# Kernel tuning notes

Hardware: AMD Instinct MI355X
Metric: run time of the kernel (lower is better)

## Reference

```python
import jax, jax.numpy as jnp
import numpy as np

BATCH, SEQ, FEAT, LAYERS = 32, 512, 1024, 2


def setup_inputs() -> dict:
    key = jax.random.key(0)
    ks = jax.random.split(key, 1 + 3 * LAYERS)
    inp = {"x": jax.random.normal(ks[0], (BATCH, SEQ, FEAT), dtype=jnp.float32)}
    scale_i = 1.0 / np.sqrt(FEAT)
    for l in range(LAYERS):
        # flax OptimizedLSTMCell: input dense (no bias) + hidden dense (with bias),
        # both producing 4*features (gates i, f, g, o concatenated).
        inp[f"Wi{l}"] = jax.random.normal(ks[1 + 3 * l], (FEAT, 4 * FEAT), dtype=jnp.float32) * scale_i
        inp[f"Wh{l}"] = jax.random.normal(ks[2 + 3 * l], (FEAT, 4 * FEAT), dtype=jnp.float32) * scale_i
        inp[f"b{l}"] = jnp.zeros((4 * FEAT,), dtype=jnp.float32)
    return inp


def _lstm_layer(x, Wi, Wh, b):
    # x: [B, T, F_in]; returns [B, T, F]
    B = x.shape[0]
    F = Wh.shape[0]
    # Precompute input projections for all steps (one big GEMM): [B, T, 4F]
    xz = jnp.einsum("btf,fg->btg", x, Wi) + b

    def step(carry, xz_t):
        c, h = carry
        z = xz_t + h @ Wh  # [B, 4F]
        i, f, g, o = jnp.split(z, 4, axis=-1)
        c_new = jax.nn.sigmoid(f) * c + jax.nn.sigmoid(i) * jnp.tanh(g)
        h_new = jax.nn.sigmoid(o) * jnp.tanh(c_new)
        return (c_new, h_new), h_new

    init = (jnp.zeros((B, F), x.dtype), jnp.zeros((B, F), x.dtype))
    _, ys = jax.lax.scan(step, init, jnp.swapaxes(xz, 0, 1))  # scan over time
    return jnp.swapaxes(ys, 0, 1)


def reference(x, Wi0, Wh0, b0, Wi1, Wh1, b1):
    y = _lstm_layer(x, Wi0, Wh0, b0)
    y = _lstm_layer(y, Wi1, Wh1, b1)
    return y
```

## Files before the change

kernel.cpp:

```cpp
#include <hip/hip_runtime.h>
#include <hip/hip_bf16.h>
#include <hip/hip_fp16.h>


typedef _Float16 f16x8 __attribute__((ext_vector_type(8)));
typedef __fp16 fp16x2 __attribute__((ext_vector_type(2)));
typedef float f32x4 __attribute__((ext_vector_type(4)));

#define NB 32
#define NTT 512
#define NF 1024
#define NG 4096
#define TFE (NTT * NF)
#define NWG 256
#define NTHR 512

#define W_F16X8 8192
#define W_BYTES (W_F16X8 * 16)
#define ZQSEG 33
#define Z_FLOATS (8 * 16 * ZQSEG)
#define LDS_BYTES (W_BYTES + Z_FLOATS * 4)
#define RINGB 65536
#define DEPTH 8
#define MBOX 4096

#define LOG2E 1.44269504f

__device__ __forceinline__ float sigm(float v) {
  return __builtin_amdgcn_rcpf(1.0f + __builtin_amdgcn_exp2f(-LOG2E * v));
}
__device__ __forceinline__ float tanh_s(float v) {
  return 2.0f * __builtin_amdgcn_rcpf(1.0f + __builtin_amdgcn_exp2f(-2.0f * LOG2E * v)) - 1.0f;
}

__device__ __forceinline__ unsigned pk(float a, float b) {
  union { fp16x2 h2; unsigned u; } c;
  c.h2 = __builtin_amdgcn_cvt_pkrtz(a, b);
  return c.u;
}

__device__ __forceinline__ f16x8 cvt8(f32x4 lo, f32x4 hi) {
  union { unsigned u[4]; f16x8 h8; } u;
  u.u[0] = pk(lo[0], lo[1]);
  u.u[1] = pk(lo[2], lo[3]);
  u.u[2] = pk(hi[0], hi[1]);
  u.u[3] = pk(hi[2], hi[3]);
  return u.h8;
}

__device__ __forceinline__ void ld4(f16x8 o[4], const char* p) {
  asm volatile("global_load_dwordx4 %0, %4, off sc0 sc1\n\t"
               "global_load_dwordx4 %1, %4, off offset:64 sc0 sc1\n\t"
               "global_load_dwordx4 %2, %4, off offset:128 sc0 sc1\n\t"
               "global_load_dwordx4 %3, %4, off offset:192 sc0 sc1"
               : "=&v"(o[0]), "=&v"(o[1]), "=&v"(o[2]), "=&v"(o[3])
               : "v"(p) : "memory");
}

__global__ __launch_bounds__(NTHR, 1) void lstm_persist(
    const float* __restrict__ x,
    const float* __restrict__ Wi0, const float* __restrict__ Wh0, const float* __restrict__ bv0,
    const float* __restrict__ Wi1, const float* __restrict__ Wh1, const float* __restrict__ bv1,
    float* __restrict__ out, unsigned short* __restrict__ hring_u16,
    unsigned* __restrict__ bar) {
  extern __shared__ char lds[];
  f16x8* Wl = (f16x8*)lds;
  float* Zr = (float*)(lds + W_BYTES);

  const int wg = blockIdx.x;
  const int tid = threadIdx.x;
  const int role = wg >> 7;
  const int fg = wg & 127;
  const int fbase = fg * 8;
  const int w = tid >> 6;
  const int Kq = w >> 1;
  const int mt = w & 1;
  const int lane = tid & 63;
  const int lr = lane & 15;
  const int g = lane >> 4;
  const bool master = (fg == 0);
  unsigned gen = 0;

  auto arrive = [&]() {
    asm volatile("s_waitcnt vmcnt(0) lgkmcnt(0)" ::: "memory");
    __syncthreads();
    ++gen;
    if (tid == 0)
      asm volatile("global_store_dword %0, %1, off sc0 sc1"
                   :: "v"(&bar[wg * 16]), "v"(gen) : "memory");
    if (master) {
      if (tid < 64) {
        const unsigned* fa = &bar[(role * 128 + 2 * tid) * 16];
        const unsigned* fb = &bar[(role * 128 + 2 * tid + 1) * 16];
        asm volatile("L%=:\n\t"
                     "global_load_dword v20, %0, off sc0 sc1\n\t"
                     "global_load_dword v21, %1, off sc0 sc1\n\t"
                     "s_waitcnt vmcnt(0)\n\t"
                     "v_cmp_lt_u32 vcc, v20, %2\n\t"
                     "s_mov_b64 s[14:15], vcc\n\t"
                     "v_cmp_lt_u32 vcc, v21, %2\n\t"
                     "s_or_b64 vcc, vcc, s[14:15]\n\t"
                     "s_cbranch_vccnz L%="
                     :: "v"(fa), "v"(fb), "v"(gen)
                     : "memory", "v20", "v21", "vcc", "s14", "s15");
      }
      __syncthreads();
      if (tid < 256)
        asm volatile("global_store_dword %0, %1, off sc0 sc1"
                     :: "v"(&bar[MBOX + tid * 16 + role]), "v"(gen) : "memory");
    }
  };

  auto waitAB = [&](unsigned minA, unsigned minB) {
    const unsigned* mb = &bar[MBOX + wg * 16];
    asm volatile("L%=:\n\t"
                 "global_load_dwordx2 v[20:21], %0, off sc0 sc1\n\t"
                 "s_waitcnt vmcnt(0)\n\t"
                 "v_cmp_lt_u32 vcc, v20, %1\n\t"
                 "s_mov_b64 s[14:15], vcc\n\t"
                 "v_cmp_lt_u32 vcc, v21, %2\n\t"
                 "s_or_b64 vcc, vcc, s[14:15]\n\t"
                 "s_cbranch_vccnz L%="
                 :: "v"(mb), "v"(minA), "v"(minB)
                 : "memory", "v20", "v21", "vcc", "s14", "s15");
  };

  const float* Wi = role ? Wi1 : Wi0;
  const float* Wh = role ? Wh1 : Wh0;
  const float* bv = role ? bv1 : bv0;
  char* h0b = (char*)hring_u16;
  char* h1b = (char*)hring_u16 + DEPTH * RINGB;
  unsigned* hmine = (unsigned*)(role ? h1b : h0b);

  for (int idx = tid; idx < 16384; idx += NTHR) {
    const int k = idx >> 3, chunk = idx & 7;
    const int q = chunk >> 1, half = chunk & 1;
    const float* src = (k < NF) ? (Wi + (size_t)k * NG) : (Wh + (size_t)(k - NF) * NG);
    const f32x4 v = *(const f32x4*)(src + q * NF + fbase + half * 4);
    const int s = k >> 5, kg = (k >> 3) & 3, jj = k & 7;
#pragma unroll
    for (int j = 0; j < 4; ++j) {
      const int c = q * 8 + half * 4 + j;
      _Float16* dst = (_Float16*)&Wl[((s * 2 + (c >> 4)) * 64) + kg * 16 + (c & 15)];
      dst[jj] = (_Float16)v[j];
    }
  }
  if (tid < 128) {
    const int b = tid >> 2, fp = tid & 3;
    __hip_atomic_store(&hmine[b * 512 + (fbase >> 1) + fp], 0u,
                       __ATOMIC_RELAXED, __HIP_MEMORY_SCOPE_AGENT);
  }
  float bias[4][2];
  if (tid < 128) {
    const int fp = tid & 3;
#pragma unroll
    for (int q = 0; q < 4; ++q) {
      bias[q][0] = bv[q * NF + fbase + 2 * fp];
      bias[q][1] = bv[q * NF + fbase + 2 * fp + 1];
    }
  }
  float cst[2] = {0.f, 0.f};
  __syncthreads();
  arrive();
  waitAB(1, 1);

  const int nrounds = role ? (NTT + 3) : NTT;
  for (int rd = 0; rd < nrounds; ++rd) {
    const bool doit = role == 0 ? true : (rd >= 3);
    const int t = role == 0 ? rd : rd - 3;

    if (doit) {
      f32x4 acc0 = {0.f, 0.f, 0.f, 0.f}, acc1 = {0.f, 0.f, 0.f, 0.f};
      const int brow = mt * 16 + lr;

      if (role == 0 && w < 4) {
        const float* xp = x + (size_t)brow * TFE + (size_t)t * NF + Kq * 512 + g * 8;
#pragma unroll
        for (int ks = 0; ks < 16; ++ks) {
          const int s = Kq * 16 + ks;
          const f32x4 al = *(const f32x4*)(xp + ks * 32);
          const f32x4 ah = *(const f32x4*)(xp + ks * 32 + 4);
          const f16x8 A = cvt8(al, ah);
          acc0 = __builtin_amdgcn_mfma_f32_16x16x32_f16(A, Wl[(s * 2 + 0) * 64 + lane], acc0, 0, 0, 0);
          acc1 = __builtin_amdgcn_mfma_f32_16x16x32_f16(A, Wl[(s * 2 + 1) * 64 + lane], acc1, 0, 0, 0);
        }
      } else {
        unsigned minA = 0, minB = 0;
        const char* hp;
        if (role == 0) {
          minA = rd + 1;
          minB = (rd >= 4) ? (unsigned)(rd - 3) : 0u;
          hp = h0b + (size_t)(rd & 7) * RINGB + brow * 2048
               + ((Kq - 2) * 512 + g * 8) * 2;
        } else if (Kq < 2) {
          minA = rd - 1;
          hp = h0b + (size_t)((rd - 2) & 7) * RINGB + brow * 2048
               + (Kq * 512 + g * 8) * 2;
        } else {
          minB = (rd == 3) ? 1u : (unsigned)(rd + 1);
          hp = h1b + (size_t)((rd - 3) & 7) * RINGB + brow * 2048
               + ((Kq - 2) * 512 + g * 8) * 2;
        }
        waitAB(minA, minB);

        f16x8 T[16];
        ld4(T + 0, hp);       ld4(T + 4, hp + 256);
        ld4(T + 8, hp + 512); ld4(T + 12, hp + 768);
        asm volatile("s_waitcnt vmcnt(12)" ::: "memory");
        __builtin_amdgcn_sched_barrier(0);
#pragma unroll
        for (int kk = 0; kk < 4; ++kk) {
          const int s = Kq * 16 + kk;
          acc0 = __builtin_amdgcn_mfma_f32_16x16x32_f16(T[kk], Wl[(s * 2 + 0) * 64 + lane], acc0, 0, 0, 0);
          acc1 = __builtin_amdgcn_mfma_f32_16x16x32_f16(T[kk], Wl[(s * 2 + 1) * 64 + lane], acc1, 0, 0, 0);
        }
        asm volatile("s_waitcnt vmcnt(8)" ::: "memory");
        __builtin_amdgcn_sched_barrier(0);
#pragma unroll
        for (int kk = 0; kk < 4; ++kk) {
          const int s = Kq * 16 + 4 + kk;
          acc0 = __builtin_amdgcn_mfma_f32_16x16x32_f16(T[4 + kk], Wl[(s * 2 + 0) * 64 + lane], acc0, 0, 0, 0);
          acc1 = __builtin_amdgcn_mfma_f32_16x16x32_f16(T[4 + kk], Wl[(s * 2 + 1) * 64 + lane], acc1, 0, 0, 0);
        }
        asm volatile("s_waitcnt vmcnt(4)" ::: "memory");
        __builtin_amdgcn_sched_barrier(0);
#pragma unroll
        for (int kk = 0; kk < 4; ++kk) {
          const int s = Kq * 16 + 8 + kk;
          acc0 = __builtin_amdgcn_mfma_f32_16x16x32_f16(T[8 + kk], Wl[(s * 2 + 0) * 64 + lane], acc0, 0, 0, 0);
          acc1 = __builtin_amdgcn_mfma_f32_16x16x32_f16(T[8 + kk], Wl[(s * 2 + 1) * 64 + lane], acc1, 0, 0, 0);
        }
        asm volatile("s_waitcnt vmcnt(0)" ::: "memory");
        __builtin_amdgcn_sched_barrier(0);
#pragma unroll
        for (int kk = 0; kk < 4; ++kk) {
          const int s = Kq * 16 + 12 + kk;
          acc0 = __builtin_amdgcn_mfma_f32_16x16x32_f16(T[12 + kk], Wl[(s * 2 + 0) * 64 + lane], acc0, 0, 0, 0);
          acc1 = __builtin_amdgcn_mfma_f32_16x16x32_f16(T[12 + kk], Wl[(s * 2 + 1) * 64 + lane], acc1, 0, 0, 0);
        }
      }

      {
        float* zb = Zr + (size_t)w * 16 * ZQSEG;
#pragma unroll
        for (int reg = 0; reg < 4; ++reg) {
          zb[(g * 4 + reg) * ZQSEG + lr] = acc0[reg];
          zb[(g * 4 + reg) * ZQSEG + 16 + lr] = acc1[reg];
        }
      }
    }
    __syncthreads();

    if (doit && tid < 128) {
      const int b = tid >> 2, fp = tid & 3;
      const int bmt = b >> 4, row = b & 15;
      float hv[2];
#pragma unroll
      for (int e = 0; e < 2; ++e) {
        const int f = 2 * fp + e;
        float zq[4];
#pragma unroll
        for (int q = 0; q < 4; ++q) {
          const int c = q * 8 + f;
          float sum = bias[q][e];
#pragma unroll
          for (int kq = 0; kq < 4; ++kq)
            sum += Zr[((kq * 2 + bmt) * 16 + row) * ZQSEG + c];
          zq[q] = sum;
        }
        const float cn = sigm(zq[1]) * cst[e] + sigm(zq[0]) * tanh_s(zq[2]);
        hv[e] = sigm(zq[3]) * tanh_s(cn);
        cst[e] = cn;
      }
      const int wslot = (t + 1) & 7;
      __hip_atomic_store(&hmine[(size_t)wslot * (RINGB / 4) + b * 512 + (fbase >> 1) + fp],
                         pk(hv[0], hv[1]), __ATOMIC_RELAXED, __HIP_MEMORY_SCOPE_AGENT);
      if (role == 1)
        *(float2*)(out + (size_t)b * TFE + (size_t)t * NF + fbase + 2 * fp) =
            make_float2(hv[0], hv[1]);
    }
    arrive();
  }
}

extern "C" void kernel_launch(void* const* d_in, const int* in_sizes, int n_in,
                              void* d_out, int out_size, void* d_ws, size_t ws_size,
                              hipStream_t stream) {
  (void)in_sizes; (void)n_in; (void)out_size; (void)ws_size;
  const float* x   = (const float*)d_in[0];
  const float* Wi0 = (const float*)d_in[1];
  const float* Wh0 = (const float*)d_in[2];
  const float* b0  = (const float*)d_in[3];
  const float* Wi1 = (const float*)d_in[4];
  const float* Wh1 = (const float*)d_in[5];
  const float* b1  = (const float*)d_in[6];
  float* out = (float*)d_out;

  unsigned short* hring = (unsigned short*)d_ws;
  unsigned* bar = (unsigned*)((char*)d_ws + 2 * DEPTH * RINGB);

  (void)hipMemsetAsync(bar, 0, 32768, stream);

  (void)hipFuncSetAttribute((const void*)lstm_persist,
                            hipFuncAttributeMaxDynamicSharedMemorySize, LDS_BYTES);

  lstm_persist<<<dim3(NWG), dim3(NTHR), LDS_BYTES, stream>>>(
      x, Wi0, Wh0, b0, Wi1, Wh1, b1, out, hring, bar);
}
```

Before: 3.782 ms.

## Shrink workgroups to two waves, drop LDS reduction and per-wave barriers

Workgroups drop from 512 to 128 threads. Each wave now covers the full K range for its 16 batch rows instead of splitting K across four waves, which removes the LDS partial-sum reduction and the __syncthreads inside each step. The gate nonlinearity runs directly on MFMA accumulators, using a lane shuffle to pair the gate columns, and h is written back as fp16 shorts. Barrier arrival becomes per wave, so the master polls 256 flags per role. Each wave now does four times the serial MFMA chain and loads per step, which lengthens per-step latency on the critical recurrent path.

```diff
diff --git a/kernel.cpp b/kernel.cpp
--- a/kernel.cpp
+++ b/kernel.cpp
@@ -13,17 +13,13 @@
 #define NG 4096
 #define TFE (NTT * NF)
 #define NWG 256
-#define NTHR 512
-
-#define W_F16X8 8192
-#define W_BYTES (W_F16X8 * 16)
-#define ZQSEG 33
-#define Z_FLOATS (8 * 16 * ZQSEG)
-#define LDS_BYTES (W_BYTES + Z_FLOATS * 4)
+#define NTHR 128
+
+#define W_BYTES 131072
+#define LDS_BYTES W_BYTES
 #define RINGB 65536
 #define DEPTH 8
-#define MBOX 4096
-
+#define MBOX 8192
 #define LOG2E 1.44269504f
 
 __device__ __forceinline__ float sigm(float v) {
@@ -65,49 +61,50 @@
     unsigned* __restrict__ bar) {
   extern __shared__ char lds[];
   f16x8* Wl = (f16x8*)lds;
-  float* Zr = (float*)(lds + W_BYTES);
 
   const int wg = blockIdx.x;
   const int tid = threadIdx.x;
   const int role = wg >> 7;
   const int fg = wg & 127;
   const int fbase = fg * 8;
-  const int w = tid >> 6;
-  const int Kq = w >> 1;
-  const int mt = w & 1;
+  const int mt = tid >> 6;
   const int lane = tid & 63;
-  const int lr = lane & 15;
+  const int n = lane & 15;
   const int g = lane >> 4;
-  const bool master = (fg == 0);
   unsigned gen = 0;
 
   auto arrive = [&]() {
     asm volatile("s_waitcnt vmcnt(0) lgkmcnt(0)" ::: "memory");
-    __syncthreads();
     ++gen;
-    if (tid == 0)
+    if (lane == 0)
       asm volatile("global_store_dword %0, %1, off sc0 sc1"
-                   :: "v"(&bar[wg * 16]), "v"(gen) : "memory");
-    if (master) {
-      if (tid < 64) {
-        const unsigned* fa = &bar[(role * 128 + 2 * tid) * 16];
-        const unsigned* fb = &bar[(role * 128 + 2 * tid + 1) * 16];
-        asm volatile("L%=:\n\t"
-                     "global_load_dword v20, %0, off sc0 sc1\n\t"
-                     "global_load_dword v21, %1, off sc0 sc1\n\t"
-                     "s_waitcnt vmcnt(0)\n\t"
-                     "v_cmp_lt_u32 vcc, v20, %2\n\t"
-                     "s_mov_b64 s[14:15], vcc\n\t"
-                     "v_cmp_lt_u32 vcc, v21, %2\n\t"
-                     "s_or_b64 vcc, vcc, s[14:15]\n\t"
-                     "s_cbranch_vccnz L%="
-                     :: "v"(fa), "v"(fb), "v"(gen)
-                     : "memory", "v20", "v21", "vcc", "s14", "s15");
-      }
-      __syncthreads();
-      if (tid < 256)
+                   :: "v"(&bar[(wg * 2 + mt) * 16]), "v"(gen) : "memory");
+    if (fg == 0 && mt == 0) {
+      const unsigned* f0 = &bar[(role * 256 + lane * 4 + 0) * 16];
+      const unsigned* f1 = &bar[(role * 256 + lane * 4 + 1) * 16];
+      const unsigned* f2 = &bar[(role * 256 + lane * 4 + 2) * 16];
+      const unsigned* f3 = &bar[(role * 256 + lane * 4 + 3) * 16];
+      asm volatile("L%=:\n\t"
+                   "global_load_dword v20, %0, off sc0 sc1\n\t"
+                   "global_load_dword v21, %1, off sc0 sc1\n\t"
+                   "global_load_dword v22, %2, off sc0 sc1\n\t"
+                   "global_load_dword v23, %3, off sc0 sc1\n\t"
+                   "s_waitcnt vmcnt(0)\n\t"
+                   "v_cmp_lt_u32 vcc, v20, %4\n\t"
+                   "s_mov_b64 s[14:15], vcc\n\t"
+                   "v_cmp_lt_u32 vcc, v21, %4\n\t"
+                   "s_or_b64 s[14:15], vcc, s[14:15]\n\t"
+                   "v_cmp_lt_u32 vcc, v22, %4\n\t"
+                   "s_or_b64 s[14:15], vcc, s[14:15]\n\t"
+                   "v_cmp_lt_u32 vcc, v23, %4\n\t"
+                   "s_or_b64 vcc, vcc, s[14:15]\n\t"
+                   "s_cbranch_vccnz L%="
+                   :: "v"(f0), "v"(f1), "v"(f2), "v"(f3), "v"(gen)
+                   : "memory", "v20", "v21", "v22", "v23", "vcc", "s14", "s15");
+#pragma unroll
+      for (int j = 0; j < 4; ++j)
         asm volatile("global_store_dword %0, %1, off sc0 sc1"
-                     :: "v"(&bar[MBOX + tid * 16 + role]), "v"(gen) : "memory");
+                     :: "v"(&bar[MBOX + (lane * 4 + j) * 16 + role]), "v"(gen) : "memory");
     }
   };
 
@@ -130,7 +127,7 @@
   const float* bv = role ? bv1 : bv0;
   char* h0b = (char*)hring_u16;
   char* h1b = (char*)hring_u16 + DEPTH * RINGB;
-  unsigned* hmine = (unsigned*)(role ? h1b : h0b);
+  char* hmine = role ? h1b : h0b;
 
   for (int idx = tid; idx < 16384; idx += NTHR) {
     const int k = idx >> 3, chunk = idx & 7;
@@ -145,24 +142,56 @@
       dst[jj] = (_Float16)v[j];
     }
   }
-  if (tid < 128) {
+  {
     const int b = tid >> 2, fp = tid & 3;
-    __hip_atomic_store(&hmine[b * 512 + (fbase >> 1) + fp], 0u,
+    __hip_atomic_store((unsigned*)hmine + b * 512 + (fbase >> 1) + fp, 0u,
                        __ATOMIC_RELAXED, __HIP_MEMORY_SCOPE_AGENT);
   }
-  float bias[4][2];
-  if (tid < 128) {
-    const int fp = tid & 3;
-#pragma unroll
-    for (int q = 0; q < 4; ++q) {
-      bias[q][0] = bv[q * NF + fbase + 2 * fp];
-      bias[q][1] = bv[q * NF + fbase + 2 * fp + 1];
-    }
-  }
-  float cst[2] = {0.f, 0.f};
+  float bq[4];
+#pragma unroll
+  for (int q = 0; q < 4; ++q) bq[q] = bv[q * NF + fbase + (lane & 7)];
+  float cst[4] = {0.f, 0.f, 0.f, 0.f};
   __syncthreads();
   arrive();
   waitAB(1, 1);
+
+  auto hphase = [&](const char* hp, int sbase, f32x4& a0, f32x4& a1) {
+    f16x8 T[32];
+#pragma unroll
+    for (int q = 0; q < 8; ++q) ld4(T + q * 4, hp + q * 256);
+    asm volatile("s_waitcnt vmcnt(24)" ::: "memory");
+    __builtin_amdgcn_sched_barrier(0);
+#pragma unroll
+    for (int kk = 0; kk < 8; ++kk) {
+      const int s = sbase + kk;
+      a0 = __builtin_amdgcn_mfma_f32_16x16x32_f16(T[kk], Wl[(s * 2 + 0) * 64 + lane], a0, 0, 0, 0);
+      a1 = __builtin_amdgcn_mfma_f32_16x16x32_f16(T[kk], Wl[(s * 2 + 1) * 64 + lane], a1, 0, 0, 0);
+    }
+    asm volatile("s_waitcnt vmcnt(16)" ::: "memory");
+    __builtin_amdgcn_sched_barrier(0);
+#pragma unroll
+    for (int kk = 8; kk < 16; ++kk) {
+      const int s = sbase + kk;
+      a0 = __builtin_amdgcn_mfma_f32_16x16x32_f16(T[kk], Wl[(s * 2 + 0) * 64 + lane], a0, 0, 0, 0);
+      a1 = __builtin_amdgcn_mfma_f32_16x16x32_f16(T[kk], Wl[(s * 2 + 1) * 64 + lane], a1, 0, 0, 0);
+    }
+    asm volatile("s_waitcnt vmcnt(8)" ::: "memory");
+    __builtin_amdgcn_sched_barrier(0);
+#pragma unroll
+    for (int kk = 16; kk < 24; ++kk) {
+      const int s = sbase + kk;
+      a0 = __builtin_amdgcn_mfma_f32_16x16x32_f16(T[kk], Wl[(s * 2 + 0) * 64 + lane], a0, 0, 0, 0);
+      a1 = __builtin_amdgcn_mfma_f32_16x16x32_f16(T[kk], Wl[(s * 2 + 1) * 64 + lane], a1, 0, 0, 0);
+    }
+    asm volatile("s_waitcnt vmcnt(0)" ::: "memory");
+    __builtin_amdgcn_sched_barrier(0);
+#pragma unroll
+    for (int kk = 24; kk < 32; ++kk) {
+      const int s = sbase + kk;
+      a0 = __builtin_amdgcn_mfma_f32_16x16x32_f16(T[kk], Wl[(s * 2 + 0) * 64 + lane], a0, 0, 0, 0);
+      a1 = __builtin_amdgcn_mfma_f32_16x16x32_f16(T[kk], Wl[(s * 2 + 1) * 64 + lane], a1, 0, 0, 0);
+    }
+  };
 
   const int nrounds = role ? (NTT + 3) : NTT;
   for (int rd = 0; rd < nrounds; ++rd) {
@@ -170,114 +199,55 @@
     const int t = role == 0 ? rd : rd - 3;
 
     if (doit) {
-      f32x4 acc0 = {0.f, 0.f, 0.f, 0.f}, acc1 = {0.f, 0.f, 0.f, 0.f};
-      const int brow = mt * 16 + lr;
-
-      if (role == 0 && w < 4) {
-        const float* xp = x + (size_t)brow * TFE + (size_t)t * NF + Kq * 512 + g * 8;
-#pragma unroll
-        for (int ks = 0; ks < 16; ++ks) {
-          const int s = Kq * 16 + ks;
+      f32x4 a0 = {0.f, 0.f, 0.f, 0.f}, a1 = {0.f, 0.f, 0.f, 0.f};
+      const int brow = mt * 16 + n;
+
+      if (role == 0) {
+        const float* xp = x + (size_t)brow * TFE + (size_t)t * NF + g * 8;
+#pragma unroll 8
+        for (int ks = 0; ks < 32; ++ks) {
           const f32x4 al = *(const f32x4*)(xp + ks * 32);
           const f32x4 ah = *(const f32x4*)(xp + ks * 32 + 4);
           const f16x8 A = cvt8(al, ah);
-          acc0 = __builtin_amdgcn_mfma_f32_16x16x32_f16(A, Wl[(s * 2 + 0) * 64 + lane], acc0, 0, 0, 0);
-          acc1 = __builtin_amdgcn_mfma_f32_16x16x32_f16(A, Wl[(s * 2 + 1) * 64 + lane], acc1, 0, 0, 0);
+          a0 = __builtin_amdgcn_mfma_f32_16x16x32_f16(A, Wl[(ks * 2 + 0) * 64 + lane], a0, 0, 0, 0);
+          a1 = __builtin_amdgcn_mfma_f32_16x16x32_f16(A, Wl[(ks * 2 + 1) * 64 + lane], a1, 0, 0, 0);
         }
+        const unsigned minB = (rd >= 4) ? (unsigned)(rd - 3) : 0u;
+        waitAB(rd + 1, minB);
+        hphase(h0b + (size_t)(rd & 7) * RINGB + brow * 2048 + g * 16, 32, a0, a1);
       } else {
-        unsigned minA = 0, minB = 0;
-        const char* hp;
-        if (role == 0) {
-          minA = rd + 1;
-          minB = (rd >= 4) ? (unsigned)(rd - 3) : 0u;
-          hp = h0b + (size_t)(rd & 7) * RINGB + brow * 2048
-               + ((Kq - 2) * 512 + g * 8) * 2;
-        } else if (Kq < 2) {
-          minA = rd - 1;
-          hp = h0b + (size_t)((rd - 2) & 7) * RINGB + brow * 2048
-               + (Kq * 512 + g * 8) * 2;
-        } else {
-          minB = (rd == 3) ? 1u : (unsigned)(rd + 1);
-          hp = h1b + (size_t)((rd - 3) & 7) * RINGB + brow * 2048
-               + ((Kq - 2) * 512 + g * 8) * 2;
-        }
-        waitAB(minA, minB);
-
-        f16x8 T[16];
-        ld4(T + 0, hp);       ld4(T + 4, hp + 256);
-        ld4(T + 8, hp + 512); ld4(T + 12, hp + 768);
-        asm volatile("s_waitcnt vmcnt(12)" ::: "memory");
-        __builtin_amdgcn_sched_barrier(0);
-#pragma unroll
-        for (int kk = 0; kk < 4; ++kk) {
-          const int s = Kq * 16 + kk;
-          acc0 = __builtin_amdgcn_mfma_f32_16x16x32_f16(T[kk], Wl[(s * 2 + 0) * 64 + lane], acc0, 0, 0, 0);
-          acc1 = __builtin_amdgcn_mfma_f32_16x16x32_f16(T[kk], Wl[(s * 2 + 1) * 64 + lane], acc1, 0, 0, 0);
-        }
-        asm volatile("s_waitcnt vmcnt(8)" ::: "memory");
-        __builtin_amdgcn_sched_barrier(0);
-#pragma unroll
-        for (int kk = 0; kk < 4; ++kk) {
-          const int s = Kq * 16 + 4 + kk;
-          acc0 = __builtin_amdgcn_mfma_f32_16x16x32_f16(T[4 + kk], Wl[(s * 2 + 0) * 64 + lane], acc0, 0, 0, 0);
-          acc1 = __builtin_amdgcn_mfma_f32_16x16x32_f16(T[4 + kk], Wl[(s * 2 + 1) * 64 + lane], acc1, 0, 0, 0);
-        }
-        asm volatile("s_waitcnt vmcnt(4)" ::: "memory");
-        __builtin_amdgcn_sched_barrier(0);
-#pragma unroll
-        for (int kk = 0; kk < 4; ++kk) {
-          const int s = Kq * 16 + 8 + kk;
-          acc0 = __builtin_amdgcn_mfma_f32_16x16x32_f16(T[8 + kk], Wl[(s * 2 + 0) * 64 + lane], acc0, 0, 0, 0);
-          acc1 = __builtin_amdgcn_mfma_f32_16x16x32_f16(T[8 + kk], Wl[(s * 2 + 1) * 64 + lane], acc1, 0, 0, 0);
-        }
-        asm volatile("s_waitcnt vmcnt(0)" ::: "memory");
-        __builtin_amdgcn_sched_barrier(0);
-#pragma unroll
-        for (int kk = 0; kk < 4; ++kk) {
-          const int s = Kq * 16 + 12 + kk;
-          acc0 = __builtin_amdgcn_mfma_f32_16x16x32_f16(T[12 + kk], Wl[(s * 2 + 0) * 64 + lane], acc0, 0, 0, 0);
-          acc1 = __builtin_amdgcn_mfma_f32_16x16x32_f16(T[12 + kk], Wl[(s * 2 + 1) * 64 + lane], acc1, 0, 0, 0);
+        waitAB(rd - 1, 0);
+        hphase(h0b + (size_t)((rd - 2) & 7) * RINGB + brow * 2048 + g * 16, 0, a0, a1);
+        const unsigned minB = (rd == 3) ? 1u : (unsigned)(rd + 1);
+        waitAB(0, minB);
+        hphase(h1b + (size_t)((rd - 3) & 7) * RINGB + brow * 2048 + g * 16, 32, a0, a1);
+      }
+
+      float o0[4], o1[4];
+#pragma unroll
+      for (int r = 0; r < 4; ++r) {
+        o0[r] = __shfl_xor(a0[r], 8, 64);
+        o1[r] = __shfl_xor(a1[r], 8, 64);
+      }
+      if (n < 8) {
+        char* hdst = hmine + (size_t)((t + 1) & 7) * RINGB;
+#pragma unroll
+        for (int r = 0; r < 4; ++r) {
+          const float zi = a0[r] + bq[0];
+          const float zf = o0[r] + bq[1];
+          const float zg = a1[r] + bq[2];
+          const float zo = o1[r] + bq[3];
+          const float cn = sigm(zf) * cst[r] + sigm(zi) * tanh_s(zg);
+          const float hv = sigm(zo) * tanh_s(cn);
+          cst[r] = cn;
+          const int b = mt * 16 + g * 4 + r;
+          const unsigned hu = pk(hv, hv);
+          asm volatile("global_store_short %0, %1, off sc0 sc1"
+                       :: "v"(hdst + b * 2048 + (fbase + n) * 2), "v"(hu) : "memory");
+          if (role == 1)
+            out[(size_t)b * TFE + (size_t)t * NF + fbase + n] = hv;
         }
       }
-
-      {
-        float* zb = Zr + (size_t)w * 16 * ZQSEG;
-#pragma unroll
-        for (int reg = 0; reg < 4; ++reg) {
-          zb[(g * 4 + reg) * ZQSEG + lr] = acc0[reg];
-          zb[(g * 4 + reg) * ZQSEG + 16 + lr] = acc1[reg];
-        }
-      }
-    }
-    __syncthreads();
-
-    if (doit && tid < 128) {
-      const int b = tid >> 2, fp = tid & 3;
-      const int bmt = b >> 4, row = b & 15;
-      float hv[2];
-#pragma unroll
-      for (int e = 0; e < 2; ++e) {
-        const int f = 2 * fp + e;
-        float zq[4];
-#pragma unroll
-        for (int q = 0; q < 4; ++q) {
-          const int c = q * 8 + f;
-          float sum = bias[q][e];
-#pragma unroll
-          for (int kq = 0; kq < 4; ++kq)
-            sum += Zr[((kq * 2 + bmt) * 16 + row) * ZQSEG + c];
-          zq[q] = sum;
-        }
-        const float cn = sigm(zq[1]) * cst[e] + sigm(zq[0]) * tanh_s(zq[2]);
-        hv[e] = sigm(zq[3]) * tanh_s(cn);
-        cst[e] = cn;
-      }
-      const int wslot = (t + 1) & 7;
-      __hip_atomic_store(&hmine[(size_t)wslot * (RINGB / 4) + b * 512 + (fbase >> 1) + fp],
-                         pk(hv[0], hv[1]), __ATOMIC_RELAXED, __HIP_MEMORY_SCOPE_AGENT);
-      if (role == 1)
-        *(float2*)(out + (size_t)b * TFE + (size_t)t * NF + fbase + 2 * fp) =
-            make_float2(hv[0], hv[1]);
     }
     arrive();
   }
@@ -299,7 +269,7 @@
   unsigned short* hring = (unsigned short*)d_ws;
   unsigned* bar = (unsigned*)((char*)d_ws + 2 * DEPTH * RINGB);
 
-  (void)hipMemsetAsync(bar, 0, 32768, stream);
+  (void)hipMemsetAsync(bar, 0, 49152, stream);
 
   (void)hipFuncSetAttribute((const void*)lstm_persist,
                             hipFuncAttributeMaxDynamicSharedMemorySize, LDS_BYTES);
```

Result: slower. 8.110 ms (+114.4%).

## Replace global barrier with sentinel-based data-flow polling on the h ring

Applied to the files above, without the earlier changes.

Removes the per-step grid barrier (arrive plus master fan-in and mailbox broadcast). Consumers instead poll the h ring buffer itself and retry until no sentinel values remain. Layer-1 workgroups reset consumed slots to the sentinel and publish a progress counter, which layer-0 polls to bound how far it runs ahead. This is meant to cut the multi-hop barrier latency on the serial recurrence, at the cost of more polling traffic and a subtle memory-ordering protocol that relies on the 32-bit h stores being atomic.

```diff
diff --git a/kernel.cpp b/kernel.cpp
--- a/kernel.cpp
+++ b/kernel.cpp
@@ -6,6 +6,7 @@
 typedef _Float16 f16x8 __attribute__((ext_vector_type(8)));
 typedef __fp16 fp16x2 __attribute__((ext_vector_type(2)));
 typedef float f32x4 __attribute__((ext_vector_type(4)));
+typedef unsigned u32x4 __attribute__((ext_vector_type(4)));
 
 #define NB 32
 #define NTT 512
@@ -15,15 +16,13 @@
 #define NWG 256
 #define NTHR 512
 
-#define W_F16X8 8192
-#define W_BYTES (W_F16X8 * 16)
+#define W_BYTES 131072
 #define ZQSEG 33
 #define Z_FLOATS (8 * 16 * ZQSEG)
 #define LDS_BYTES (W_BYTES + Z_FLOATS * 4)
 #define RINGB 65536
-#define DEPTH 8
-#define MBOX 4096
-
+#define RINGU (RINGB / 4)
+#define SENT 0xFFFFFFFFu
 #define LOG2E 1.44269504f
 
 __device__ __forceinline__ float sigm(float v) {
@@ -55,6 +54,25 @@
                "global_load_dwordx4 %3, %4, off offset:192 sc0 sc1"
                : "=&v"(o[0]), "=&v"(o[1]), "=&v"(o[2]), "=&v"(o[3])
                : "v"(p) : "memory");
+}
+
+__device__ __forceinline__ void pollge(const unsigned* p, unsigned thr) {
+  asm volatile("L%=:\n\t"
+               "global_load_dword v20, %0, off sc0 sc1\n\t"
+               "s_waitcnt vmcnt(0)\n\t"
+               "v_cmp_lt_u32 vcc, v20, %1\n\t"
+               "s_cbranch_vccnz L%="
+               :: "v"(p), "v"(thr) : "memory", "v20", "vcc");
+}
+
+__device__ __forceinline__ int grp_ok(const f16x8* Tg) {
+  int ok = 1;
+#pragma unroll
+  for (int j = 0; j < 4; ++j) {
+    const u32x4 v = __builtin_bit_cast(u32x4, Tg[j]);
+    ok &= (v.x != SENT) & (v.y != SENT) & (v.z != SENT) & (v.w != SENT);
+  }
+  return ok;
 }
 
 __global__ __launch_bounds__(NTHR, 1) void lstm_persist(
@@ -78,59 +96,41 @@
   const int lane = tid & 63;
   const int lr = lane & 15;
   const int g = lane >> 4;
-  const bool master = (fg == 0);
-  unsigned gen = 0;
-
-  auto arrive = [&]() {
-    asm volatile("s_waitcnt vmcnt(0) lgkmcnt(0)" ::: "memory");
-    __syncthreads();
-    ++gen;
-    if (tid == 0)
-      asm volatile("global_store_dword %0, %1, off sc0 sc1"
-                   :: "v"(&bar[wg * 16]), "v"(gen) : "memory");
-    if (master) {
-      if (tid < 64) {
-        const unsigned* fa = &bar[(role * 128 + 2 * tid) * 16];
-        const unsigned* fb = &bar[(role * 128 + 2 * tid + 1) * 16];
-        asm volatile("L%=:\n\t"
-                     "global_load_dword v20, %0, off sc0 sc1\n\t"
-                     "global_load_dword v21, %1, off sc0 sc1\n\t"
-                     "s_waitcnt vmcnt(0)\n\t"
-                     "v_cmp_lt_u32 vcc, v20, %2\n\t"
-                     "s_mov_b64 s[14:15], vcc\n\t"
-                     "v_cmp_lt_u32 vcc, v21, %2\n\t"
-                     "s_or_b64 vcc, vcc, s[14:15]\n\t"
-                     "s_cbranch_vccnz L%="
-                     :: "v"(fa), "v"(fb), "v"(gen)
-                     : "memory", "v20", "v21", "vcc", "s14", "s15");
-      }
-      __syncthreads();
-      if (tid < 256)
-        asm volatile("global_store_dword %0, %1, off sc0 sc1"
-                     :: "v"(&bar[MBOX + tid * 16 + role]), "v"(gen) : "memory");
-    }
-  };
-
-  auto waitAB = [&](unsigned minA, unsigned minB) {
-    const unsigned* mb = &bar[MBOX + wg * 16];
-    asm volatile("L%=:\n\t"
-                 "global_load_dwordx2 v[20:21], %0, off sc0 sc1\n\t"
-                 "s_waitcnt vmcnt(0)\n\t"
-                 "v_cmp_lt_u32 vcc, v20, %1\n\t"
-                 "s_mov_b64 s[14:15], vcc\n\t"
-                 "v_cmp_lt_u32 vcc, v21, %2\n\t"
-                 "s_or_b64 vcc, vcc, s[14:15]\n\t"
-                 "s_cbranch_vccnz L%="
-                 :: "v"(mb), "v"(minA), "v"(minB)
-                 : "memory", "v20", "v21", "vcc", "s14", "s15");
-  };
 
   const float* Wi = role ? Wi1 : Wi0;
   const float* Wh = role ? Wh1 : Wh0;
   const float* bv = role ? bv1 : bv0;
   char* h0b = (char*)hring_u16;
-  char* h1b = (char*)hring_u16 + DEPTH * RINGB;
-  unsigned* hmine = (unsigned*)(role ? h1b : h0b);
+  char* h1b = (char*)hring_u16 + 8 * RINGB;
+  unsigned* hmu = (unsigned*)(role ? h1b : h0b);
+
+  auto hphase = [&](const char* hp, int sbase, f32x4& a0, f32x4& a1) {
+    f16x8 T[16];
+    ld4(T + 0, hp);       ld4(T + 4, hp + 256);
+    ld4(T + 8, hp + 512); ld4(T + 12, hp + 768);
+    asm volatile("s_waitcnt vmcnt(0)" ::: "memory");
+    __builtin_amdgcn_sched_barrier(0);
+    if (!__all(grp_ok(T) & grp_ok(T + 4) & grp_ok(T + 8) & grp_ok(T + 12))) {
+      for (;;) {
+        ld4(T + 0, hp);
+        asm volatile("s_waitcnt vmcnt(0)" ::: "memory");
+        __builtin_amdgcn_sched_barrier(0);
+        if (__all(grp_ok(T))) break;
+      }
+      for (;;) {
+        ld4(T + 4, hp + 256); ld4(T + 8, hp + 512); ld4(T + 12, hp + 768);
+        asm volatile("s_waitcnt vmcnt(0)" ::: "memory");
+        __builtin_amdgcn_sched_barrier(0);
+        if (__all(grp_ok(T + 4) & grp_ok(T + 8) & grp_ok(T + 12))) break;
+      }
+    }
+#pragma unroll
+    for (int kk = 0; kk < 16; ++kk) {
+      const int s = sbase + kk;
+      a0 = __builtin_amdgcn_mfma_f32_16x16x32_f16(T[kk], Wl[(s * 2 + 0) * 64 + lane], a0, 0, 0, 0);
+      a1 = __builtin_amdgcn_mfma_f32_16x16x32_f16(T[kk], Wl[(s * 2 + 1) * 64 + lane], a1, 0, 0, 0);
+    }
+  };
 
   for (int idx = tid; idx < 16384; idx += NTHR) {
     const int k = idx >> 3, chunk = idx & 7;
@@ -147,8 +147,12 @@
   }
   if (tid < 128) {
     const int b = tid >> 2, fp = tid & 3;
-    __hip_atomic_store(&hmine[b * 512 + (fbase >> 1) + fp], 0u,
-                       __ATOMIC_RELAXED, __HIP_MEMORY_SCOPE_AGENT);
+    unsigned* up = hmu + b * 512 + fg * 4 + fp;
+    __hip_atomic_store(up, 0u, __ATOMIC_RELAXED, __HIP_MEMORY_SCOPE_AGENT);
+#pragma unroll
+    for (int s = 1; s < 8; ++s)
+      __hip_atomic_store(up + (size_t)s * RINGU, SENT,
+                         __ATOMIC_RELAXED, __HIP_MEMORY_SCOPE_AGENT);
   }
   float bias[4][2];
   if (tid < 128) {
@@ -160,9 +164,13 @@
     }
   }
   float cst[2] = {0.f, 0.f};
+
+  asm volatile("s_waitcnt vmcnt(0) lgkmcnt(0)\ns_barrier" ::: "memory");
+  if (tid == 0)
+    asm volatile("global_store_dword %0, %1, off sc0 sc1"
+                 :: "v"(&bar[wg * 16]), "v"(1u) : "memory");
+  if (tid < 256) pollge(&bar[tid * 16], 1u);
   __syncthreads();
-  arrive();
-  waitAB(1, 1);
 
   const int nrounds = role ? (NTT + 3) : NTT;
   for (int rd = 0; rd < nrounds; ++rd) {
@@ -170,86 +178,44 @@
     const int t = role == 0 ? rd : rd - 3;
 
     if (doit) {
-      f32x4 acc0 = {0.f, 0.f, 0.f, 0.f}, acc1 = {0.f, 0.f, 0.f, 0.f};
+      f32x4 a0 = {0.f, 0.f, 0.f, 0.f}, a1 = {0.f, 0.f, 0.f, 0.f};
       const int brow = mt * 16 + lr;
 
-      if (role == 0 && w < 4) {
-        const float* xp = x + (size_t)brow * TFE + (size_t)t * NF + Kq * 512 + g * 8;
-#pragma unroll
-        for (int ks = 0; ks < 16; ++ks) {
-          const int s = Kq * 16 + ks;
-          const f32x4 al = *(const f32x4*)(xp + ks * 32);
-          const f32x4 ah = *(const f32x4*)(xp + ks * 32 + 4);
-          const f16x8 A = cvt8(al, ah);
-          acc0 = __builtin_amdgcn_mfma_f32_16x16x32_f16(A, Wl[(s * 2 + 0) * 64 + lane], acc0, 0, 0, 0);
-          acc1 = __builtin_amdgcn_mfma_f32_16x16x32_f16(A, Wl[(s * 2 + 1) * 64 + lane], acc1, 0, 0, 0);
+      if (role == 0) {
+        if (Kq < 2) {
+          if (w < 2 && rd >= 4)
+            pollge(&bar[(128 + (tid & 127)) * 16], (unsigned)rd - 2);
+          const float* xp = x + (size_t)brow * TFE + (size_t)t * NF + Kq * 512 + g * 8;
+#pragma unroll
+          for (int ks = 0; ks < 16; ++ks) {
+            const int s = Kq * 16 + ks;
+            const f32x4 al = *(const f32x4*)(xp + ks * 32);
+            const f32x4 ah = *(const f32x4*)(xp + ks * 32 + 4);
+            const f16x8 A = cvt8(al, ah);
+            a0 = __builtin_amdgcn_mfma_f32_16x16x32_f16(A, Wl[(s * 2 + 0) * 64 + lane], a0, 0, 0, 0);
+            a1 = __builtin_amdgcn_mfma_f32_16x16x32_f16(A, Wl[(s * 2 + 1) * 64 + lane], a1, 0, 0, 0);
+          }
+        } else {
+          hphase(h0b + (size_t)(rd & 7) * RINGB + brow * 2048 + ((Kq - 2) * 512 + g * 8) * 2,
+                 Kq * 16, a0, a1);
         }
       } else {
-        unsigned minA = 0, minB = 0;
-        const char* hp;
-        if (role == 0) {
-          minA = rd + 1;
-          minB = (rd >= 4) ? (unsigned)(rd - 3) : 0u;
-          hp = h0b + (size_t)(rd & 7) * RINGB + brow * 2048
-               + ((Kq - 2) * 512 + g * 8) * 2;
-        } else if (Kq < 2) {
-          minA = rd - 1;
-          hp = h0b + (size_t)((rd - 2) & 7) * RINGB + brow * 2048
-               + (Kq * 512 + g * 8) * 2;
-        } else {
-          minB = (rd == 3) ? 1u : (unsigned)(rd + 1);
-          hp = h1b + (size_t)((rd - 3) & 7) * RINGB + brow * 2048
-               + ((Kq - 2) * 512 + g * 8) * 2;
-        }
-        waitAB(minA, minB);
-
-        f16x8 T[16];
-        ld4(T + 0, hp);       ld4(T + 4, hp + 256);
-        ld4(T + 8, hp + 512); ld4(T + 12, hp + 768);
-        asm volatile("s_waitcnt vmcnt(12)" ::: "memory");
-        __builtin_amdgcn_sched_barrier(0);
-#pragma unroll
-        for (int kk = 0; kk < 4; ++kk) {
-          const int s = Kq * 16 + kk;
-          acc0 = __builtin_amdgcn_mfma_f32_16x16x32_f16(T[kk], Wl[(s * 2 + 0) * 64 + lane], acc0, 0, 0, 0);
-          acc1 = __builtin_amdgcn_mfma_f32_16x16x32_f16(T[kk], Wl[(s * 2 + 1) * 64 + lane], acc1, 0, 0, 0);
-        }
-        asm volatile("s_waitcnt vmcnt(8)" ::: "memory");
-        __builtin_amdgcn_sched_barrier(0);
-#pragma unroll
-        for (int kk = 0; kk < 4; ++kk) {
-          const int s = Kq * 16 + 4 + kk;
-          acc0 = __builtin_amdgcn_mfma_f32_16x16x32_f16(T[4 + kk], Wl[(s * 2 + 0) * 64 + lane], acc0, 0, 0, 0);
-          acc1 = __builtin_amdgcn_mfma_f32_16x16x32_f16(T[4 + kk], Wl[(s * 2 + 1) * 64 + lane], acc1, 0, 0, 0);
-        }
-        asm volatile("s_waitcnt vmcnt(4)" ::: "memory");
-        __builtin_amdgcn_sched_barrier(0);
-#pragma unroll
-        for (int kk = 0; kk < 4; ++kk) {
-          const int s = Kq * 16 + 8 + kk;
-          acc0 = __builtin_amdgcn_mfma_f32_16x16x32_f16(T[8 + kk], Wl[(s * 2 + 0) * 64 + lane], acc0, 0, 0, 0);
-          acc1 = __builtin_amdgcn_mfma_f32_16x16x32_f16(T[8 + kk], Wl[(s * 2 + 1) * 64 + lane], acc1, 0, 0, 0);
-        }
-        asm volatile("s_waitcnt vmcnt(0)" ::: "memory");
-        __builtin_amdgcn_sched_barrier(0);
-#pragma unroll
-        for (int kk = 0; kk < 4; ++kk) {
-          const int s = Kq * 16 + 12 + kk;
-          acc0 = __builtin_amdgcn_mfma_f32_16x16x32_f16(T[12 + kk], Wl[(s * 2 + 0) * 64 + lane], acc0, 0, 0, 0);
-          acc1 = __builtin_amdgcn_mfma_f32_16x16x32_f16(T[12 + kk], Wl[(s * 2 + 1) * 64 + lane], acc1, 0, 0, 0);
-        }
-      }
-
-      {
-        float* zb = Zr + (size_t)w * 16 * ZQSEG;
-#pragma unroll
-        for (int reg = 0; reg < 4; ++reg) {
-          zb[(g * 4 + reg) * ZQSEG + lr] = acc0[reg];
-          zb[(g * 4 + reg) * ZQSEG + 16 + lr] = acc1[reg];
-        }
-      }
-    }
-    __syncthreads();
+        if (Kq < 2)
+          hphase(h0b + (size_t)((rd - 2) & 7) * RINGB + brow * 2048 + (Kq * 512 + g * 8) * 2,
+                 Kq * 16, a0, a1);
+        else
+          hphase(h1b + (size_t)((rd - 3) & 7) * RINGB + brow * 2048 + ((Kq - 2) * 512 + g * 8) * 2,
+                 Kq * 16, a0, a1);
+      }
+
+      float* zb = Zr + (size_t)w * 16 * ZQSEG;
+#pragma unroll
+      for (int reg = 0; reg < 4; ++reg) {
+        zb[(g * 4 + reg) * ZQSEG + lr] = a0[reg];
+        zb[(g * 4 + reg) * ZQSEG + 16 + lr] = a1[reg];
+      }
+    }
+    asm volatile("s_waitcnt lgkmcnt(0)\ns_barrier" ::: "memory");
 
     if (doit && tid < 128) {
       const int b = tid >> 2, fp = tid & 3;
@@ -272,14 +238,28 @@
         hv[e] = sigm(zq[3]) * tanh_s(cn);
         cst[e] = cn;
       }
-      const int wslot = (t + 1) & 7;
-      __hip_atomic_store(&hmine[(size_t)wslot * (RINGB / 4) + b * 512 + (fbase >> 1) + fp],
+      __hip_atomic_store(hmu + (size_t)((t + 1) & 7) * RINGU + b * 512 + fg * 4 + fp,
                          pk(hv[0], hv[1]), __ATOMIC_RELAXED, __HIP_MEMORY_SCOPE_AGENT);
-      if (role == 1)
+      if (role == 1) {
         *(float2*)(out + (size_t)b * TFE + (size_t)t * NF + fbase + 2 * fp) =
             make_float2(hv[0], hv[1]);
-    }
-    arrive();
+        pollge(&bar[(128 + tid) * 16], (unsigned)rd + 1);
+        __hip_atomic_store((unsigned*)h0b + (size_t)((rd - 3) & 7) * RINGU + b * 512 + fg * 4 + fp,
+                           SENT, __ATOMIC_RELAXED, __HIP_MEMORY_SCOPE_AGENT);
+        if (rd >= 4)
+          __hip_atomic_store((unsigned*)h1b + (size_t)((rd - 4) & 7) * RINGU + b * 512 + fg * 4 + fp,
+                             SENT, __ATOMIC_RELAXED, __HIP_MEMORY_SCOPE_AGENT);
+      }
+    }
+
+    if (role == 1) {
+      asm volatile("s_waitcnt vmcnt(0) lgkmcnt(0)\ns_barrier" ::: "memory");
+      if (tid == 0)
+        asm volatile("global_store_dword %0, %1, off sc0 sc1"
+                     :: "v"(&bar[wg * 16]), "v"((unsigned)(rd + 2)) : "memory");
+    } else {
+      asm volatile("s_waitcnt lgkmcnt(0)\ns_barrier" ::: "memory");
+    }
   }
 }
 
@@ -297,9 +277,9 @@
   float* out = (float*)d_out;
 
   unsigned short* hring = (unsigned short*)d_ws;
-  unsigned* bar = (unsigned*)((char*)d_ws + 2 * DEPTH * RINGB);
-
-  (void)hipMemsetAsync(bar, 0, 32768, stream);
+  unsigned* bar = (unsigned*)((char*)d_ws + 16 * RINGB);
+
+  (void)hipMemsetAsync(bar, 0, 16384, stream);
 
   (void)hipFuncSetAttribute((const void*)lstm_persist,
                             hipFuncAttributeMaxDynamicSharedMemorySize, LDS_BYTES);
```

Measured after the change: 5.163 ms. 36.5% more time.
